# Optimization experiments

Measured on AMD Instinct MI355X. Metric: run time of the kernel, lower is better.

## Reference

```python
import jax, jax.numpy as jnp
import numpy as np


def _perceive(x):
    """Depthwise 3x3 perception: per channel emit (identity, dx, dy), matching
    tf.nn.depthwise_conv2d with kernel repeated along the in-channel axis, so
    output channel ordering is [c0_I, c0_dx, c0_dy, c1_I, ...]."""
    C = x.shape[-1]
    _i = jnp.array([0.0, 1.0, 0.0], dtype=x.dtype)
    I = jnp.outer(_i, _i)
    dx = jnp.outer(jnp.array([1.0, 2.0, 1.0], dtype=x.dtype),
                   jnp.array([-1.0, 0.0, 1.0], dtype=x.dtype)) / 8.0
    dy = dx.T
    base = jnp.stack([I, dx, dy], axis=-1)[:, :, None, :]  # [3,3,1,3]
    kernel = jnp.tile(base, (1, 1, 1, C))                   # [3,3,1,3C]
    # grouped conv with feature_group_count=C == depthwise conv, multiplier 3
    y = jax.lax.conv_general_dilated(
        x, kernel, window_strides=(1, 1), padding='SAME',
        dimension_numbers=('NHWC', 'HWIO', 'NHWC'), feature_group_count=C)
    return y  # [B,H,W,3C]


def setup_inputs() -> dict:
    key = jax.random.key(0)
    ks = jax.random.split(key, 6)
    B, H, W, C = 16, 256, 256, 16
    x = jax.random.normal(ks[0], (B, H, W, C), dtype=jnp.float32)
    # update mask: tf.random.normal(...) <= fire_rate (0.5), per pixel
    update_mask = jax.random.normal(ks[1], (B, H, W, 1), dtype=jnp.float32) <= 0.5
    # 1x1 conv weights (glorot-ish scale). NOTE: the original zero-initializes
    # w3/b3; we use small random values so the op is numerically non-trivial.
    w1 = jax.random.normal(ks[2], (3 * C, 4 * C), dtype=jnp.float32) / np.sqrt(3 * C)
    b1 = jnp.zeros((4 * C,), dtype=jnp.float32)
    w2 = jax.random.normal(ks[3], (4 * C, 2 * C), dtype=jnp.float32) / np.sqrt(4 * C)
    b2 = jnp.zeros((2 * C,), dtype=jnp.float32)
    w3 = jax.random.normal(ks[4], (2 * C, C), dtype=jnp.float32) / np.sqrt(2 * C)
    b3 = jnp.zeros((C,), dtype=jnp.float32)
    return {"x": x, "w1": w1, "b1": b1, "w2": w2, "b2": b2,
            "w3": w3, "b3": b3, "update_mask": update_mask}


def reference(x, w1, b1, w2, b2, w3, b3, update_mask):
    step_size = 1.0
    y = _perceive(x)  # [B,H,W,3C]
    h = jnp.tanh(jnp.einsum('bhwc,cd->bhwd', y, w1) + b1)
    h = jnp.tanh(jnp.einsum('bhwc,cd->bhwd', h, w2) + b2)
    dx = (jnp.einsum('bhwc,cd->bhwd', h, w3) + b3) * step_size
    return x + dx * update_mask.astype(x.dtype)
```

## Files before the change

### kernel.cpp

```cpp
#include <hip/hip_runtime.h>
#include <hip/hip_bf16.h>

typedef unsigned int u32;
typedef unsigned short u16;
typedef unsigned char u8;

typedef float f32x16 __attribute__((ext_vector_type(16)));
typedef short bf16x8 __attribute__((ext_vector_type(8)));

#define OFF_A1  0
#define OFF_A1B 18432
#define OFF_WT2 20480
#define OFF_WT3 25600
#define OFF_B3  27648
#define PREP_N  13840

__device__ __forceinline__ float bf2f(u16 h) {
  return __uint_as_float(((u32)h) << 16);
}
__device__ __forceinline__ u16 f2bf(float f) {
  u32 u = __float_as_uint(f);
  return (u16)((u + 0x7FFFu + ((u >> 16) & 1u)) >> 16);
}
__device__ __forceinline__ u32 pkbf(float a, float b) {
  u32 r;
  asm("v_cvt_pk_bf16_f32 %0, %1, %2" : "=v"(r) : "v"(a), "v"(b));
  return r;
}
__device__ __forceinline__ float rdv(const void* s, int i, bool bf) {
  return bf ? bf2f(((const u16*)s)[i]) : ((const float*)s)[i];
}

__global__ void prep_weights(const void* __restrict__ w1, const void* __restrict__ b1,
                             const void* __restrict__ w2, const void* __restrict__ b2,
                             const void* __restrict__ w3, const void* __restrict__ b3,
                             u8* __restrict__ Wb) {
  __shared__ int sg;
  if (threadIdx.x == 0) sg = 0;
  __syncthreads();
  {
    const u16* w1h = (const u16*)w1;
    int g = 0;
#pragma unroll
    for (int k = 0; k < 8; ++k) {
      u16 h = w1h[threadIdx.x * 8 + k];
      int e = (h >> 7) & 0xFF;
      if (e >= 0xC0) g++;
    }
    if (g) atomicAdd(&sg, g);
  }
  __syncthreads();
  const bool bf = (sg == 0);

  int i = blockIdx.x * 256 + threadIdx.x;
  if (i >= PREP_N) return;
  if (i < 9216) {
    int off = i >> 10, rem = i & 1023;
    int mt = rem >> 9, hi = (rem >> 8) & 1, l = (rem >> 3) & 31, k8 = i & 7;
    int ch = mt * 32 + l, k = hi * 8 + k8;
    int oi = off / 3, oj = off % 3;
    const float axv[3] = {1.f, 2.f, 1.f};
    const float bxv[3] = {-1.f, 0.f, 1.f};
    float ci  = (oi == 1 && oj == 1) ? 1.f : 0.f;
    float dxv = axv[oi] * bxv[oj] * 0.125f;
    float dyv = axv[oj] * bxv[oi] * 0.125f;
    float v = ci  * rdv(w1, (3 * k + 0) * 64 + ch, bf)
            + dxv * rdv(w1, (3 * k + 1) * 64 + ch, bf)
            + dyv * rdv(w1, (3 * k + 2) * 64 + ch, bf);
    ((u16*)(Wb + OFF_A1))[i] = f2bf(v);
  } else if (i < 10240) {
    int j = i - 9216;
    int mt = j >> 9, l = (j >> 3) & 31;
    ((u16*)(Wb + OFF_A1B))[j] = f2bf(rdv(b1, mt * 32 + l, bf) * 0.0625f);
  } else if (i < 12800) {
    int j = i - 10240, n = j / 80, k = j - n * 80;
    float v;
    if (k < 64) {
      int s = k >> 4, hh = (k >> 3) & 1, q = (k & 7) >> 1, e = k & 1;
      int c = 32 * (s >> 1) + 8 * (2 * (s & 1) + (q >> 1)) + 4 * hh + 2 * (q & 1) + e;
      v = rdv(w2, c * 32 + n, bf);
    } else {
      v = (k == 64) ? rdv(b2, n, bf) : 0.0f;
    }
    ((u16*)(Wb + OFF_WT2))[j] = f2bf(v);
  } else if (i < 13824) {
    int j = i - 12800, n = j >> 5, k = j & 31;
    float v = 0.0f;
    if (n < 16) {
      int cout = (n & 3) + 4 * ((n >> 3) & 1) + 8 * ((n >> 2) & 1);
      int s = k >> 4, hh = (k >> 3) & 1, q = (k & 7) >> 1, e = k & 1;
      int cin = 8 * (2 * s + (q >> 1)) + 4 * hh + 2 * (q & 1) + e;
      v = rdv(w3, cin * 16 + cout, bf);
    }
    ((u16*)(Wb + OFF_WT3))[j] = f2bf(v);
  } else {
    int j = i - 13824;
    ((float*)(Wb + OFF_B3))[j] = rdv(b3, j, bf);
  }
}

__device__ __forceinline__ float fast_tanh(float x) {
  float e = __builtin_amdgcn_exp2f(x * 2.8853900817779268f);
  float r = __builtin_amdgcn_rcpf(e + 1.0f);
  return fmaf(-2.0f, r, 1.0f);
}

union U4 { uint4 q; u32 u[4]; bf16x8 h; float4 f; };

__device__ __forceinline__ void wave_lds_fence() {
  __builtin_amdgcn_wave_barrier();
  __asm__ __volatile__("s_waitcnt lgkmcnt(0)" ::: "memory");
  __builtin_amdgcn_wave_barrier();
}

#define MFMA(a, b, c) __builtin_amdgcn_mfma_f32_32x32x16_bf16((a), (b), (c), 0, 0, 0)

#define XS_STRIDE 8256
#define SCR_OFF   33024
#define SCR_WAVE  2560
#define LDS_TOTAL 43264

template <bool BF16>
__device__ __forceinline__ void nca_body(const void* __restrict__ xv,
                                         const u8* __restrict__ Wb,
                                         const void* __restrict__ maskv, int mw,
                                         void* __restrict__ outv,
                                         u8* __restrict__ xs) {
  const int tid = threadIdx.x;
  const int l   = tid & 63;
  const int wid = tid >> 6;
  const int l31 = l & 31;
  const int hi  = l >> 5;
  const int img   = blockIdx.x >> 7;
  const int r0    = (blockIdx.x & 127) << 1;

  if (tid < 8) {
    int rr = tid >> 1, side = tid & 1;
    uint4 z = make_uint4(0, 0, 0, 0);
    uint4* d = (uint4*)(xs + rr * XS_STRIDE + (side ? 257 : 0) * 32);
    d[0] = z; d[1] = z;
  }
#pragma unroll
  for (int rr = 0; rr < 4; ++rr) {
    int hr = r0 - 1 + rr;
    bool valid = (hr >= 0) && (hr <= 255);
    if (BF16) {
      const u16* src = (const u16*)xv + ((size_t)(img * 256 + hr) << 12);
#pragma unroll
      for (int s = 0; s < 2; ++s) {
        int c = s * 256 + tid;
        uint4 v = make_uint4(0, 0, 0, 0);
        if (valid) v = *(const uint4*)(src + c * 8);
        *(uint4*)(xs + rr * XS_STRIDE + ((c >> 1) + 1) * 32 + (c & 1) * 16) = v;
      }
    } else {
      const float* src = (const float*)xv + ((size_t)(img * 256 + hr) << 12);
#pragma unroll
      for (int k = 0; k < 4; ++k) {
        int q = k * 256 + tid;
        uint2 w = make_uint2(0, 0);
        if (valid) {
          float4 v = *(const float4*)(src + q * 4);
          w.x = pkbf(v.x, v.y); w.y = pkbf(v.z, v.w);
        }
        *(uint2*)(xs + rr * XS_STRIDE + ((q >> 2) + 1) * 32 + (q & 3) * 8) = w;
      }
    }
  }
  __syncthreads();

  const int sr      = wid >> 1;
  const int colbase = (wid & 1) * 128;
  const int gr      = img * 256 + r0 + sr;
  const int growpix = gr << 8;

  bf16x8 A1b[2];
#pragma unroll
  for (int mt = 0; mt < 2; ++mt) {
    U4 t; t.q = *(const uint4*)(Wb + OFF_A1B + ((mt * 2 + hi) * 32 + l31) * 16);
    A1b[mt] = t.h;
  }
  U4 ones; ones.u[0] = ones.u[1] = ones.u[2] = ones.u[3] = 0x3F803F80u;
  const float* B3f = (const float*)(Wb + OFF_B3);
  float4 b3lo = *(const float4*)(B3f + 8 * hi);
  float4 b3hi4 = *(const float4*)(B3f + 8 * hi + 4);
  u8* scr = xs + SCR_OFF + wid * SCR_WAVE;

  bf16x8 A2h[5], A3h[2];
#pragma unroll
  for (int s = 0; s < 5; ++s) {
    U4 t; t.q = *(const uint4*)(Wb + OFF_WT2 + l31 * 160 + s * 32 + hi * 16);
    A2h[s] = t.h;
  }
#pragma unroll
  for (int s = 0; s < 2; ++s) {
    U4 t; t.q = *(const uint4*)(Wb + OFF_WT3 + l31 * 64 + s * 32 + hi * 16);
    A3h[s] = t.h;
  }
  U4 bbf; bbf.u[0] = hi ? 0u : 0x00003F80u; bbf.u[1] = 0; bbf.u[2] = 0; bbf.u[3] = 0;

  const int ep_px = l >> 2;
  const int ep_qd = l & 3;

#pragma unroll
  for (int t = 0; t < 4; ++t) {
    const int cb = colbase + t * 32;

    const int gpx1 = growpix + cb + ep_px;
    const int gpx2 = gpx1 + 16;
    const int e1 = gpx1 * 16 + ep_qd * 4;
    const int e2 = gpx2 * 16 + ep_qd * 4;
    bool ms1, ms2;
    if (mw == 1)      { ms1 = ((const u8*)maskv)[gpx1] != 0;  ms2 = ((const u8*)maskv)[gpx2] != 0; }
    else if (mw == 2) { ms1 = ((const u16*)maskv)[gpx1] != 0; ms2 = ((const u16*)maskv)[gpx2] != 0; }
    else              { ms1 = ((const u32*)maskv)[gpx1] != 0; ms2 = ((const u32*)maskv)[gpx2] != 0; }
    const float mf1 = ms1 ? 1.0f : 0.0f;
    const float mf2 = ms2 ? 1.0f : 0.0f;
    uint2 xu1, xu2;
    float4 xc1, xc2;
    if (BF16) {
      xu1 = *(const uint2*)((const u16*)xv + e1);
      xu2 = *(const uint2*)((const u16*)xv + e2);
    } else {
      xc1 = *(const float4*)((const float*)xv + e1);
      xc2 = *(const float4*)((const float*)xv + e2);
    }

    f32x16 c0 = {0,0,0,0,0,0,0,0,0,0,0,0,0,0,0,0};
    f32x16 c1 = {0,0,0,0,0,0,0,0,0,0,0,0,0,0,0,0};
    c0 = MFMA(A1b[0], ones.h, c0);
    c1 = MFMA(A1b[1], ones.h, c1);
#pragma unroll
    for (int off = 0; off < 9; ++off) {
      const int oi = off / 3, oj = off % 3;
      U4 bx; bx.q = *(const uint4*)(xs + (sr + oi) * XS_STRIDE +
                                    (cb + l31 + oj) * 32 + hi * 16);
      U4 a0; a0.q = *(const uint4*)(Wb + OFF_A1 + (((off * 2 + 0) * 2 + hi) * 32 + l31) * 16);
      U4 a1; a1.q = *(const uint4*)(Wb + OFF_A1 + (((off * 2 + 1) * 2 + hi) * 32 + l31) * 16);
      c0 = MFMA(a0.h, bx.h, c0);
      c1 = MFMA(a1.h, bx.h, c1);
    }

    u32 o1[16];
#pragma unroll
    for (int g = 0; g < 4; ++g)
#pragma unroll
      for (int pp = 0; pp < 2; ++pp) {
        o1[g * 2 + pp]     = pkbf(fast_tanh(c0[g * 4 + 2 * pp]), fast_tanh(c0[g * 4 + 2 * pp + 1]));
        o1[8 + g * 2 + pp] = pkbf(fast_tanh(c1[g * 4 + 2 * pp]), fast_tanh(c1[g * 4 + 2 * pp + 1]));
      }

    f32x16 c2 = {0,0,0,0,0,0,0,0,0,0,0,0,0,0,0,0};
#pragma unroll
    for (int s = 0; s < 4; ++s) {
      U4 bfr; bfr.u[0] = o1[4*s]; bfr.u[1] = o1[4*s+1]; bfr.u[2] = o1[4*s+2]; bfr.u[3] = o1[4*s+3];
      c2 = MFMA(A2h[s], bfr.h, c2);
    }
    c2 = MFMA(A2h[4], bbf.h, c2);
    u32 o2[8];
#pragma unroll
    for (int g = 0; g < 4; ++g)
#pragma unroll
      for (int pp = 0; pp < 2; ++pp)
        o2[g * 2 + pp] = pkbf(fast_tanh(c2[g * 4 + 2 * pp]), fast_tanh(c2[g * 4 + 2 * pp + 1]));

    f32x16 c3 = {0,0,0,0,0,0,0,0,0,0,0,0,0,0,0,0};
#pragma unroll
    for (int s = 0; s < 2; ++s) {
      U4 bfr; bfr.u[0] = o2[4*s]; bfr.u[1] = o2[4*s+1]; bfr.u[2] = o2[4*s+2]; bfr.u[3] = o2[4*s+3];
      c3 = MFMA(A3h[s], bfr.h, c3);
    }

    U4 w0, w1;
    w0.f.x = c3[0] + b3lo.x;  w0.f.y = c3[1] + b3lo.y;
    w0.f.z = c3[2] + b3lo.z;  w0.f.w = c3[3] + b3lo.w;
    w1.f.x = c3[4] + b3hi4.x; w1.f.y = c3[5] + b3hi4.y;
    w1.f.z = c3[6] + b3hi4.z; w1.f.w = c3[7] + b3hi4.w;
    u8* sa = scr + l31 * 80 + hi * 32;
    *(float4*)(sa) = w0.f;
    *(float4*)(sa + 16) = w1.f;
    wave_lds_fence();

    {
      float4 dx1 = *(const float4*)(scr + ep_px * 80 + ep_qd * 16);
      float4 dx2 = *(const float4*)(scr + (16 + ep_px) * 80 + ep_qd * 16);
      if (BF16) {
        float x10 = bf2f((u16)(xu1.x & 0xFFFF)), x11 = bf2f((u16)(xu1.x >> 16));
        float x12 = bf2f((u16)(xu1.y & 0xFFFF)), x13 = bf2f((u16)(xu1.y >> 16));
        float x20 = bf2f((u16)(xu2.x & 0xFFFF)), x21 = bf2f((u16)(xu2.x >> 16));
        float x22 = bf2f((u16)(xu2.y & 0xFFFF)), x23 = bf2f((u16)(xu2.y >> 16));
        uint2 wa, wb;
        wa.x = pkbf(fmaf(dx1.x, mf1, x10), fmaf(dx1.y, mf1, x11));
        wa.y = pkbf(fmaf(dx1.z, mf1, x12), fmaf(dx1.w, mf1, x13));
        wb.x = pkbf(fmaf(dx2.x, mf2, x20), fmaf(dx2.y, mf2, x21));
        wb.y = pkbf(fmaf(dx2.z, mf2, x22), fmaf(dx2.w, mf2, x23));
        *(uint2*)((u16*)outv + e1) = wa;
        *(uint2*)((u16*)outv + e2) = wb;
      } else {
        float4 oa, ob;
        oa.x = fmaf(dx1.x, mf1, xc1.x); oa.y = fmaf(dx1.y, mf1, xc1.y);
        oa.z = fmaf(dx1.z, mf1, xc1.z); oa.w = fmaf(dx1.w, mf1, xc1.w);
        ob.x = fmaf(dx2.x, mf2, xc2.x); ob.y = fmaf(dx2.y, mf2, xc2.y);
        ob.z = fmaf(dx2.z, mf2, xc2.z); ob.w = fmaf(dx2.w, mf2, xc2.w);
        *(float4*)((float*)outv + e1) = oa;
        *(float4*)((float*)outv + e2) = ob;
      }
    }
    wave_lds_fence();
  }
}

__global__ __launch_bounds__(256, 3) void nca_main(const void* __restrict__ xv,
                                                   const u16* __restrict__ w1h,
                                                   const u8* __restrict__ Wb,
                                                   const void* __restrict__ maskv,
                                                   void* __restrict__ outv) {
  __shared__ __align__(16) u8 smem[LDS_TOTAL];
  __shared__ int sg, su8, sbf;
  if (threadIdx.x == 0) { sg = 0; su8 = 0; sbf = 0; }
  __syncthreads();
  {
    int g = 0;
#pragma unroll
    for (int k = 0; k < 8; ++k) {
      u16 h = w1h[threadIdx.x * 8 + k];
      int e = (h >> 7) & 0xFF;
      if (e >= 0xC0) g++;
    }
    if (g) atomicAdd(&sg, g);
    u32 w = ((const u32*)maskv)[threadIdx.x];
    bool bytes01 = ((w & 0xFEFEFEFEu) == 0u);
    int bsum = (int)(w & 1u) + (int)((w >> 8) & 1u) +
               (int)((w >> 16) & 1u) + (int)((w >> 24) & 1u);
    if (bytes01 && bsum >= 2) atomicAdd(&su8, 1);
    if (w == 0x3F803F80u || w == 0x00003F80u) atomicAdd(&sbf, 1);
  }
  __syncthreads();
  const bool isbf = (sg == 0);
  const int mw = (su8 > 0) ? 1 : ((sbf > 0) ? 2 : 4);

  if (isbf) nca_body<true>(xv, Wb, maskv, mw, outv, smem);
  else      nca_body<false>(xv, Wb, maskv, mw, outv, smem);
}

extern "C" void kernel_launch(void* const* d_in, const int* in_sizes, int n_in,
                              void* d_out, int out_size, void* d_ws, size_t ws_size,
                              hipStream_t stream) {
  u8* Wb = (u8*)d_ws + 64;

  prep_weights<<<(PREP_N + 255) / 256, 256, 0, stream>>>(
      d_in[1], d_in[2], d_in[3], d_in[4], d_in[5], d_in[6], Wb);

  const int pixels = in_sizes[7];
  const int blocks = pixels / 512;
  nca_main<<<blocks, 256, 0, stream>>>(d_in[0], (const u16*)d_in[1], Wb,
                                       d_in[7], d_out);
}
```

Measured before the change: 177.5 us.

## Double-buffer epilogue scratch and defer each tile's output write to next iteration

Splits the per-wave LDS scratch into two buffers and software-pipelines the epilogue. Each tile's residual add and global store now run during the next tile's layer-1 MFMAs instead of after an extra LDS fence. This removes one wave-level LDS wait per tile and overlaps the store and LDS-read latency with matrix work. In exchange the LDS footprint grows, which can lower occupancy, and more values stay live in registers across iterations.

```diff
diff --git a/kernel.cpp b/kernel.cpp
--- a/kernel.cpp
+++ b/kernel.cpp
@@ -117,8 +117,9 @@
 
 #define XS_STRIDE 8256
 #define SCR_OFF   33024
-#define SCR_WAVE  2560
-#define LDS_TOTAL 43264
+#define SCR_WAVE  5120
+#define SCR_BUF   2560
+#define LDS_TOTAL 53504
 
 template <bool BF16>
 __device__ __forceinline__ void nca_body(const void* __restrict__ xv,
@@ -202,6 +203,11 @@
   const int ep_px = l >> 2;
   const int ep_qd = l & 3;
 
+  float pm1 = 0.f, pm2 = 0.f;
+  int pe1 = 0, pe2 = 0;
+  uint2 pxu1 = {0, 0}, pxu2 = {0, 0};
+  float4 pxc1 = {0,0,0,0}, pxc2 = {0,0,0,0};
+
 #pragma unroll
   for (int t = 0; t < 4; ++t) {
     const int cb = colbase + t * 32;
@@ -216,14 +222,21 @@
     else              { ms1 = ((const u32*)maskv)[gpx1] != 0; ms2 = ((const u32*)maskv)[gpx2] != 0; }
     const float mf1 = ms1 ? 1.0f : 0.0f;
     const float mf2 = ms2 ? 1.0f : 0.0f;
-    uint2 xu1, xu2;
-    float4 xc1, xc2;
+    uint2 xu1 = {0, 0}, xu2 = {0, 0};
+    float4 xc1 = {0,0,0,0}, xc2 = {0,0,0,0};
     if (BF16) {
       xu1 = *(const uint2*)((const u16*)xv + e1);
       xu2 = *(const uint2*)((const u16*)xv + e2);
     } else {
       xc1 = *(const float4*)((const float*)xv + e1);
       xc2 = *(const float4*)((const float*)xv + e2);
+    }
+
+    float4 dx1 = {0,0,0,0}, dx2 = {0,0,0,0};
+    if (t > 0) {
+      const u8* pb = scr + ((t - 1) & 1) * SCR_BUF;
+      dx1 = *(const float4*)(pb + ep_px * 80 + ep_qd * 16);
+      dx2 = *(const float4*)(pb + (16 + ep_px) * 80 + ep_qd * 16);
     }
 
     f32x16 c0 = {0,0,0,0,0,0,0,0,0,0,0,0,0,0,0,0};
@@ -241,6 +254,30 @@
       c1 = MFMA(a1.h, bx.h, c1);
     }
 
+    if (t > 0) {
+      if (BF16) {
+        float x10 = bf2f((u16)(pxu1.x & 0xFFFF)), x11 = bf2f((u16)(pxu1.x >> 16));
+        float x12 = bf2f((u16)(pxu1.y & 0xFFFF)), x13 = bf2f((u16)(pxu1.y >> 16));
+        float x20 = bf2f((u16)(pxu2.x & 0xFFFF)), x21 = bf2f((u16)(pxu2.x >> 16));
+        float x22 = bf2f((u16)(pxu2.y & 0xFFFF)), x23 = bf2f((u16)(pxu2.y >> 16));
+        uint2 wa, wb;
+        wa.x = pkbf(fmaf(dx1.x, pm1, x10), fmaf(dx1.y, pm1, x11));
+        wa.y = pkbf(fmaf(dx1.z, pm1, x12), fmaf(dx1.w, pm1, x13));
+        wb.x = pkbf(fmaf(dx2.x, pm2, x20), fmaf(dx2.y, pm2, x21));
+        wb.y = pkbf(fmaf(dx2.z, pm2, x22), fmaf(dx2.w, pm2, x23));
+        *(uint2*)((u16*)outv + pe1) = wa;
+        *(uint2*)((u16*)outv + pe2) = wb;
+      } else {
+        float4 oa, ob;
+        oa.x = fmaf(dx1.x, pm1, pxc1.x); oa.y = fmaf(dx1.y, pm1, pxc1.y);
+        oa.z = fmaf(dx1.z, pm1, pxc1.z); oa.w = fmaf(dx1.w, pm1, pxc1.w);
+        ob.x = fmaf(dx2.x, pm2, pxc2.x); ob.y = fmaf(dx2.y, pm2, pxc2.y);
+        ob.z = fmaf(dx2.z, pm2, pxc2.z); ob.w = fmaf(dx2.w, pm2, pxc2.w);
+        *(float4*)((float*)outv + pe1) = oa;
+        *(float4*)((float*)outv + pe2) = ob;
+      }
+    }
+
     u32 o1[16];
 #pragma unroll
     for (int g = 0; g < 4; ++g)
@@ -276,37 +313,40 @@
     w0.f.z = c3[2] + b3lo.z;  w0.f.w = c3[3] + b3lo.w;
     w1.f.x = c3[4] + b3hi4.x; w1.f.y = c3[5] + b3hi4.y;
     w1.f.z = c3[6] + b3hi4.z; w1.f.w = c3[7] + b3hi4.w;
-    u8* sa = scr + l31 * 80 + hi * 32;
+    u8* sa = scr + (t & 1) * SCR_BUF + l31 * 80 + hi * 32;
     *(float4*)(sa) = w0.f;
     *(float4*)(sa + 16) = w1.f;
     wave_lds_fence();
 
-    {
-      float4 dx1 = *(const float4*)(scr + ep_px * 80 + ep_qd * 16);
-      float4 dx2 = *(const float4*)(scr + (16 + ep_px) * 80 + ep_qd * 16);
-      if (BF16) {
-        float x10 = bf2f((u16)(xu1.x & 0xFFFF)), x11 = bf2f((u16)(xu1.x >> 16));
-        float x12 = bf2f((u16)(xu1.y & 0xFFFF)), x13 = bf2f((u16)(xu1.y >> 16));
-        float x20 = bf2f((u16)(xu2.x & 0xFFFF)), x21 = bf2f((u16)(xu2.x >> 16));
-        float x22 = bf2f((u16)(xu2.y & 0xFFFF)), x23 = bf2f((u16)(xu2.y >> 16));
-        uint2 wa, wb;
-        wa.x = pkbf(fmaf(dx1.x, mf1, x10), fmaf(dx1.y, mf1, x11));
-        wa.y = pkbf(fmaf(dx1.z, mf1, x12), fmaf(dx1.w, mf1, x13));
-        wb.x = pkbf(fmaf(dx2.x, mf2, x20), fmaf(dx2.y, mf2, x21));
-        wb.y = pkbf(fmaf(dx2.z, mf2, x22), fmaf(dx2.w, mf2, x23));
-        *(uint2*)((u16*)outv + e1) = wa;
-        *(uint2*)((u16*)outv + e2) = wb;
-      } else {
-        float4 oa, ob;
-        oa.x = fmaf(dx1.x, mf1, xc1.x); oa.y = fmaf(dx1.y, mf1, xc1.y);
-        oa.z = fmaf(dx1.z, mf1, xc1.z); oa.w = fmaf(dx1.w, mf1, xc1.w);
-        ob.x = fmaf(dx2.x, mf2, xc2.x); ob.y = fmaf(dx2.y, mf2, xc2.y);
-        ob.z = fmaf(dx2.z, mf2, xc2.z); ob.w = fmaf(dx2.w, mf2, xc2.w);
-        *(float4*)((float*)outv + e1) = oa;
-        *(float4*)((float*)outv + e2) = ob;
-      }
-    }
-    wave_lds_fence();
+    pm1 = mf1; pm2 = mf2; pe1 = e1; pe2 = e2;
+    pxu1 = xu1; pxu2 = xu2; pxc1 = xc1; pxc2 = xc2;
+  }
+
+  {
+    const u8* pb = scr + (3 & 1) * SCR_BUF;
+    float4 dx1 = *(const float4*)(pb + ep_px * 80 + ep_qd * 16);
+    float4 dx2 = *(const float4*)(pb + (16 + ep_px) * 80 + ep_qd * 16);
+    if (BF16) {
+      float x10 = bf2f((u16)(pxu1.x & 0xFFFF)), x11 = bf2f((u16)(pxu1.x >> 16));
+      float x12 = bf2f((u16)(pxu1.y & 0xFFFF)), x13 = bf2f((u16)(pxu1.y >> 16));
+      float x20 = bf2f((u16)(pxu2.x & 0xFFFF)), x21 = bf2f((u16)(pxu2.x >> 16));
+      float x22 = bf2f((u16)(pxu2.y & 0xFFFF)), x23 = bf2f((u16)(pxu2.y >> 16));
+      uint2 wa, wb;
+      wa.x = pkbf(fmaf(dx1.x, pm1, x10), fmaf(dx1.y, pm1, x11));
+      wa.y = pkbf(fmaf(dx1.z, pm1, x12), fmaf(dx1.w, pm1, x13));
+      wb.x = pkbf(fmaf(dx2.x, pm2, x20), fmaf(dx2.y, pm2, x21));
+      wb.y = pkbf(fmaf(dx2.z, pm2, x22), fmaf(dx2.w, pm2, x23));
+      *(uint2*)((u16*)outv + pe1) = wa;
+      *(uint2*)((u16*)outv + pe2) = wb;
+    } else {
+      float4 oa, ob;
+      oa.x = fmaf(dx1.x, pm1, pxc1.x); oa.y = fmaf(dx1.y, pm1, pxc1.y);
+      oa.z = fmaf(dx1.z, pm1, pxc1.z); oa.w = fmaf(dx1.w, pm1, pxc1.w);
+      ob.x = fmaf(dx2.x, pm2, pxc2.x); ob.y = fmaf(dx2.y, pm2, pxc2.y);
+      ob.z = fmaf(dx2.z, pm2, pxc2.z); ob.w = fmaf(dx2.w, pm2, pxc2.w);
+      *(float4*)((float*)outv + pe1) = oa;
+      *(float4*)((float*)outv + pe2) = ob;
+    }
   }
 }
 
```

New measurement: 177.6 us. Within noise of the previous version (+0.1%).
